# Performance work log

Hardware: AMD Instinct MI355X
Metric: run time of the kernel (lower is better)

## Reference

```python
import jax, jax.numpy as jnp
import numpy as np

N = 50000      # total nodes across batch of molecules
E = 1200000    # directed edges
D_IN = 9       # ESOL num_features
D = 64         # EMBEDDING_DIM
G = 1024       # number of graphs in batch


def setup_inputs() -> dict:
    key = jax.random.key(0)
    ks = jax.random.split(key, 13)
    x = jax.random.normal(ks[0], (N, D_IN), jnp.float32)
    edge_index = jax.random.randint(ks[1], (2, E), 0, N, dtype=jnp.int64)
    batch_index = jnp.sort(jax.random.randint(ks[2], (N,), 0, G, dtype=jnp.int64))

    def glorot(k, shape):
        lim = np.sqrt(6.0 / (shape[0] + shape[1])).astype(np.float32)
        return jax.random.uniform(k, shape, jnp.float32, -lim, lim)

    W0 = glorot(ks[3], (D_IN, D)); b0 = jnp.zeros((D,), jnp.float32)
    W1 = glorot(ks[4], (D, D));    b1 = jnp.zeros((D,), jnp.float32)
    W2 = glorot(ks[5], (D, D));    b2 = jnp.zeros((D,), jnp.float32)
    W3 = glorot(ks[6], (D, D));    b3 = jnp.zeros((D,), jnp.float32)
    Wout = glorot(ks[7], (2 * D, 1)); bout = jnp.zeros((1,), jnp.float32)
    return dict(x=x, edge_index=edge_index, batch_index=batch_index,
                W0=W0, b0=b0, W1=W1, b1=b1, W2=W2, b2=b2, W3=W3, b3=b3,
                Wout=Wout, bout=bout)


def _gcn_conv(h, W, b, src, dst, dinv):
    # GCNConv: D^{-1/2} (A + I) D^{-1/2} (h W) + b, with self-loops in degree.
    h = h @ W                                   # [N, D]
    norm = (dinv[src] * dinv[dst])[:, None]     # [E, 1]
    agg = jax.ops.segment_sum(h[src] * norm, dst, num_segments=N)
    agg = agg + h * (dinv * dinv)[:, None]      # self-loop contribution
    return agg + b


def reference(x, edge_index, batch_index, W0, b0, W1, b1, W2, b2, W3, b3, Wout, bout):
    src, dst = edge_index[0], edge_index[1]
    # degree over A + I (self-loops added), as in PyG GCNConv default
    deg = jax.ops.segment_sum(jnp.ones((E,), x.dtype), dst, num_segments=N) + 1.0
    dinv = jax.lax.rsqrt(deg)

    h = jnp.tanh(_gcn_conv(x, W0, b0, src, dst, dinv))
    h = jnp.tanh(_gcn_conv(h, W1, b1, src, dst, dinv))
    h = jnp.tanh(_gcn_conv(h, W2, b2, src, dst, dinv))
    h = jnp.tanh(_gcn_conv(h, W3, b3, src, dst, dinv))

    # global max pool + global mean pool per graph
    gmax = jax.ops.segment_max(h, batch_index, num_segments=G)
    gmax = jnp.where(jnp.isfinite(gmax), gmax, 0.0)   # guard empty segments
    gsum = jax.ops.segment_sum(h, batch_index, num_segments=G)
    cnt = jax.ops.segment_sum(jnp.ones((N,), h.dtype), batch_index, num_segments=G)
    gmean = gsum / jnp.maximum(cnt, 1.0)[:, None]

    hidden = jnp.concatenate([gmax, gmean], axis=1)   # [G, 2D]
    out = hidden @ Wout + bout                        # [G, 1]
    return out, hidden
```

## Files before the change

### kernel.cpp

```cpp
#include <hip/hip_runtime.h>
#include <math.h>

#define D 64

__global__ void k_zero(int* p, int n) {
    int i = blockIdx.x * blockDim.x + threadIdx.x;
    if (i < n) p[i] = 0;
}

__global__ void k_hist(const int* __restrict__ dst, int* __restrict__ counts, int e) {
    int i = blockIdx.x * blockDim.x + threadIdx.x;
    if (i < e) atomicAdd(&counts[dst[i]], 1);
}

__global__ void k_dinv(const int* __restrict__ counts, float* __restrict__ dinv, int n) {
    int i = blockIdx.x * blockDim.x + threadIdx.x;
    if (i < n) dinv[i] = rsqrtf((float)counts[i] + 1.0f);
}

__global__ void k_scan1(const int* __restrict__ counts, int* __restrict__ bsums, int n) {
    __shared__ int red[256];
    int i = blockIdx.x * 256 + threadIdx.x;
    red[threadIdx.x] = (i < n) ? counts[i] : 0;
    __syncthreads();
    for (int off = 128; off > 0; off >>= 1) {
        if (threadIdx.x < off) red[threadIdx.x] += red[threadIdx.x + off];
        __syncthreads();
    }
    if (threadIdx.x == 0) bsums[blockIdx.x] = red[0];
}

__global__ void k_scan2(int* __restrict__ bsums, int* __restrict__ rowptr, int nb, int n) {
    __shared__ int part[1024];
    int t = threadIdx.x;
    part[t] = (t < nb) ? bsums[t] : 0;
    __syncthreads();
    for (int off = 1; off < 1024; off <<= 1) {
        int v = (t >= off) ? part[t - off] : 0;
        __syncthreads();
        part[t] += v;
        __syncthreads();
    }
    if (t < nb) bsums[t] = (t == 0) ? 0 : part[t - 1];
    if (t == 1023) rowptr[n] = part[1023];
}

__global__ void k_scan3(int* __restrict__ counts, const int* __restrict__ bsums,
                        int* __restrict__ rowptr, int n) {
    __shared__ int part[256];
    int i = blockIdx.x * 256 + threadIdx.x;
    int t = threadIdx.x;
    int v = (i < n) ? counts[i] : 0;
    part[t] = v;
    __syncthreads();
    for (int off = 1; off < 256; off <<= 1) {
        int u = (t >= off) ? part[t - off] : 0;
        __syncthreads();
        part[t] += u;
        __syncthreads();
    }
    if (i < n) {
        int excl = bsums[blockIdx.x] + part[t] - v;
        rowptr[i] = excl;
        counts[i] = excl;
    }
}

__global__ void k_scatter(const int* __restrict__ src, const int* __restrict__ dst,
                          int* __restrict__ cur, int* __restrict__ ssrc, int e) {
    int i = blockIdx.x * blockDim.x + threadIdx.x;
    if (i < e) { int p = atomicAdd(&cur[dst[i]], 1); ssrc[p] = src[i]; }
}

template <int K>
__global__ void k_matmul(const float* __restrict__ h, const float* __restrict__ W,
                         const float* __restrict__ dinv, float* __restrict__ hws, int n) {
    __shared__ float sW[K * D];
    for (int i = threadIdx.x; i < K * D; i += blockDim.x) sW[i] = W[i];
    __syncthreads();
    int col = threadIdx.x & 63;
    int row = blockIdx.x * (blockDim.x >> 6) + (threadIdx.x >> 6);
    if (row >= n) return;
    const float* hr = h + (long)row * K;
    float acc = 0.0f;
#pragma unroll
    for (int k = 0; k < K; ++k) acc = fmaf(hr[k], sW[k * D + col], acc);
    hws[row * D + col] = acc * dinv[row];
}

__global__ void k_aggregate(const int* __restrict__ rowptr, const int* __restrict__ ssrc,
                            const float* __restrict__ dinv, const float* __restrict__ hws,
                            const float* __restrict__ b, float* __restrict__ hout, int n) {
    int node = blockIdx.x * (blockDim.x >> 6) + (threadIdx.x >> 6);
    int lane = threadIdx.x & 63;
    if (node >= n) return;
    int beg = rowptr[node], end = rowptr[node + 1];
    float acc = hws[node * D + lane];
    int e = beg;
    for (; e + 4 <= end; e += 4) {
        int s0 = ssrc[e], s1 = ssrc[e + 1], s2 = ssrc[e + 2], s3 = ssrc[e + 3];
        float a0 = hws[s0 * D + lane], a1 = hws[s1 * D + lane];
        float a2 = hws[s2 * D + lane], a3 = hws[s3 * D + lane];
        acc += a0; acc += a1; acc += a2; acc += a3;
    }
    for (; e < end; ++e) acc += hws[ssrc[e] * D + lane];
    hout[node * D + lane] = tanhf(acc * dinv[node] + b[lane]);
}

__global__ void k_pool(const float* __restrict__ h, const int* __restrict__ batch,
                       const float* __restrict__ Wout, const float* __restrict__ bout,
                       float* __restrict__ out, float* __restrict__ hidden, int n) {
    int g = blockIdx.x;
    int lo = 0, hi = n;
    while (lo < hi) { int mid = (lo + hi) >> 1; if (batch[mid] < g) lo = mid + 1; else hi = mid; }
    int start = lo;
    hi = n;
    while (lo < hi) { int mid = (lo + hi) >> 1; if (batch[mid] < g + 1) lo = mid + 1; else hi = mid; }
    int end = lo;

    int j = threadIdx.x;
    float mx = -INFINITY, sm = 0.0f;
    for (int nd = start; nd < end; ++nd) {
        float v = h[nd * D + j];
        mx = fmaxf(mx, v);
        sm += v;
    }
    float gmax  = (end > start) ? mx : 0.0f;
    float gmean = sm / fmaxf((float)(end - start), 1.0f);

    hidden[g * 2 * D + j]     = gmax;
    hidden[g * 2 * D + D + j] = gmean;

    float p = gmax * Wout[j] + gmean * Wout[D + j];
#pragma unroll
    for (int off = 32; off > 0; off >>= 1) p += __shfl_down(p, off, 64);
    if (j == 0) out[g] = p + bout[0];
}

extern "C" void kernel_launch(void* const* d_in, const int* in_sizes, int n_in,
                              void* d_out, int out_size, void* d_ws, size_t ws_size,
                              hipStream_t stream) {
    const float* x     = (const float*)d_in[0];
    const int*   ei    = (const int*)d_in[1];
    const int*   batch = (const int*)d_in[2];
    const float* W0 = (const float*)d_in[3];  const float* b0 = (const float*)d_in[4];
    const float* W1 = (const float*)d_in[5];  const float* b1 = (const float*)d_in[6];
    const float* W2 = (const float*)d_in[7];  const float* b2 = (const float*)d_in[8];
    const float* W3 = (const float*)d_in[9];  const float* b3 = (const float*)d_in[10];
    const float* Wout = (const float*)d_in[11];
    const float* bout = (const float*)d_in[12];
    float* out = (float*)d_out;

    const int N = in_sizes[0] / 9;
    const int E = in_sizes[1] / 2;
    const int G = out_size / (2 * D + 1);
    const int* src = ei;
    const int* dst = ei + E;
    float* hidden = out + G;

    char* ws = (char*)d_ws;
    size_t off = 0;
    auto alloc = [&](size_t bytes) { void* p = ws + off; off += (bytes + 255) & ~(size_t)255; return p; };
    int*   counts = (int*)alloc((size_t)N * sizeof(int));
    int*   rowptr = (int*)alloc((size_t)(N + 1) * sizeof(int));
    float* dinv   = (float*)alloc((size_t)N * sizeof(float));
    int*   ssrc   = (int*)alloc((size_t)E * sizeof(int));
    int*   bsums  = (int*)alloc(1024 * sizeof(int));
    float* buf0   = (float*)alloc((size_t)N * D * sizeof(float));
    float* buf1   = (float*)alloc((size_t)N * D * sizeof(float));

    const int T = 256;
    const int nb = (N + 255) / 256;

    k_zero<<<(N + T - 1) / T, T, 0, stream>>>(counts, N);
    k_hist<<<(E + T - 1) / T, T, 0, stream>>>(dst, counts, E);
    k_dinv<<<(N + T - 1) / T, T, 0, stream>>>(counts, dinv, N);
    k_scan1<<<nb, 256, 0, stream>>>(counts, bsums, N);
    k_scan2<<<1, 1024, 0, stream>>>(bsums, rowptr, nb, N);
    k_scan3<<<nb, 256, 0, stream>>>(counts, bsums, rowptr, N);
    k_scatter<<<(E + T - 1) / T, T, 0, stream>>>(src, dst, counts, ssrc, E);

    auto layer = [&](const float* hin, int K, const float* W, const float* b) {
        if (K == 9)
            k_matmul<9><<<(N + 3) / 4, T, 0, stream>>>(hin, W, dinv, buf1, N);
        else
            k_matmul<64><<<(N + 3) / 4, T, 0, stream>>>(hin, W, dinv, buf1, N);
        k_aggregate<<<(N + 3) / 4, T, 0, stream>>>(rowptr, ssrc, dinv, buf1, b, buf0, N);
    };

    layer(x,    9,  W0, b0);
    layer(buf0, 64, W1, b1);
    layer(buf0, 64, W2, b2);
    layer(buf0, 64, W3, b3);

    k_pool<<<G, 64, 0, stream>>>(buf0, batch, Wout, bout, out, hidden, N);
}
```

Measured before the change: 601.3 us.

## Build CSR via two-pass LSD radix sort of packed 16-bit dst/src keys

Replaces the atomic histogram plus atomic scatter CSR build with a stable two-pass 8-bit LSD radix sort over edges packed as (dst<<16)|src in 32-bit words. Row pointers come from a binary search on the sorted keys, and degrees are derived from them. The aggregation kernel unpacks src from the low 16 bits. The aim is to replace global atomics on random destinations with workgroup-local histograms and ballot-based ranking, and to give sorted, ordered source lists that may improve gather locality. The packing only holds when N fits in 16 bits, which N=50000 does, and the sort adds several kernel launches.

```diff
diff --git a/kernel.cpp b/kernel.cpp
--- a/kernel.cpp
+++ b/kernel.cpp
@@ -2,26 +2,34 @@
 #include <math.h>
 
 #define D 64
-
-__global__ void k_zero(int* p, int n) {
-    int i = blockIdx.x * blockDim.x + threadIdx.x;
-    if (i < n) p[i] = 0;
-}
-
-__global__ void k_hist(const int* __restrict__ dst, int* __restrict__ counts, int e) {
-    int i = blockIdx.x * blockDim.x + threadIdx.x;
-    if (i < e) atomicAdd(&counts[dst[i]], 1);
-}
-
-__global__ void k_dinv(const int* __restrict__ counts, float* __restrict__ dinv, int n) {
-    int i = blockIdx.x * blockDim.x + threadIdx.x;
-    if (i < n) dinv[i] = rsqrtf((float)counts[i] + 1.0f);
-}
-
-__global__ void k_scan1(const int* __restrict__ counts, int* __restrict__ bsums, int n) {
+#define CHUNK 8192
+#define WAVE_E 2048
+#define ITER 32
+
+
+template <int SHIFT, bool PACKED>
+__global__ void k_rhist(const void* __restrict__ keysrc, int* __restrict__ gmat,
+                        int e, int nwg) {
+    __shared__ int hist[256];
+    int t = threadIdx.x, wg = blockIdx.x;
+    hist[t] = 0;
+    __syncthreads();
+    int base = wg * CHUNK;
+    int lim = min(CHUNK, e - base);
+    for (int i = t; i < lim; i += 256) {
+        unsigned int key;
+        if (PACKED) key = ((const unsigned int*)keysrc)[base + i] >> 16;
+        else        key = (unsigned int)((const int*)keysrc)[base + i];
+        atomicAdd(&hist[(key >> SHIFT) & 255], 1);
+    }
+    __syncthreads();
+    gmat[t * nwg + wg] = hist[t];
+}
+
+__global__ void k_scanA(const int* __restrict__ a, int* __restrict__ bsums, int n) {
     __shared__ int red[256];
     int i = blockIdx.x * 256 + threadIdx.x;
-    red[threadIdx.x] = (i < n) ? counts[i] : 0;
+    red[threadIdx.x] = (i < n) ? a[i] : 0;
     __syncthreads();
     for (int off = 128; off > 0; off >>= 1) {
         if (threadIdx.x < off) red[threadIdx.x] += red[threadIdx.x + off];
@@ -29,8 +37,7 @@
     }
     if (threadIdx.x == 0) bsums[blockIdx.x] = red[0];
 }
-
-__global__ void k_scan2(int* __restrict__ bsums, int* __restrict__ rowptr, int nb, int n) {
+__global__ void k_scanB(int* __restrict__ bsums, int nb) {
     __shared__ int part[1024];
     int t = threadIdx.x;
     part[t] = (t < nb) ? bsums[t] : 0;
@@ -42,15 +49,12 @@
         __syncthreads();
     }
     if (t < nb) bsums[t] = (t == 0) ? 0 : part[t - 1];
-    if (t == 1023) rowptr[n] = part[1023];
-}
-
-__global__ void k_scan3(int* __restrict__ counts, const int* __restrict__ bsums,
-                        int* __restrict__ rowptr, int n) {
+}
+__global__ void k_scanC(int* __restrict__ a, const int* __restrict__ bsums, int n) {
     __shared__ int part[256];
     int i = blockIdx.x * 256 + threadIdx.x;
     int t = threadIdx.x;
-    int v = (i < n) ? counts[i] : 0;
+    int v = (i < n) ? a[i] : 0;
     part[t] = v;
     __syncthreads();
     for (int off = 1; off < 256; off <<= 1) {
@@ -59,17 +63,79 @@
         part[t] += u;
         __syncthreads();
     }
-    if (i < n) {
-        int excl = bsums[blockIdx.x] + part[t] - v;
-        rowptr[i] = excl;
-        counts[i] = excl;
-    }
-}
-
-__global__ void k_scatter(const int* __restrict__ src, const int* __restrict__ dst,
-                          int* __restrict__ cur, int* __restrict__ ssrc, int e) {
+    if (i < n) a[i] = bsums[blockIdx.x] + part[t] - v;
+}
+
+template <int SHIFT>
+__global__ void k_rscat(const int* __restrict__ src, const int* __restrict__ dst,
+                        const unsigned int* __restrict__ inp, const int* __restrict__ gmat,
+                        unsigned int* __restrict__ outp, int e, int nwg) {
+    __shared__ int whist[4][256];
+    __shared__ int cnt[4][256];
+    int t = threadIdx.x, wg = blockIdx.x;
+    int wave = t >> 6, lane = t & 63;
+    for (int w = 0; w < 4; ++w) whist[w][t] = 0;
+    __syncthreads();
+    int qbase = wg * CHUNK + wave * WAVE_E;
+    for (int it = 0; it < ITER; ++it) {
+        int idx = qbase + it * 64 + lane;
+        if (idx < e) {
+            unsigned int w32 = (SHIFT == 0)
+                ? (((unsigned int)dst[idx] << 16) | (unsigned int)src[idx])
+                : inp[idx];
+            atomicAdd(&whist[wave][(w32 >> (16 + SHIFT)) & 255], 1);
+        }
+    }
+    __syncthreads();
+    {
+        int g = gmat[t * nwg + wg];
+        cnt[0][t] = g;
+        g += whist[0][t]; cnt[1][t] = g;
+        g += whist[1][t]; cnt[2][t] = g;
+        g += whist[2][t]; cnt[3][t] = g;
+    }
+    __syncthreads();
+    for (int it = 0; it < ITER; ++it) {
+        int idx = qbase + it * 64 + lane;
+        bool valid = idx < e;
+        unsigned int w32 = 0; int bin = 0;
+        if (valid) {
+            w32 = (SHIFT == 0)
+                ? (((unsigned int)dst[idx] << 16) | (unsigned int)src[idx])
+                : inp[idx];
+            bin = (w32 >> (16 + SHIFT)) & 255;
+        }
+        unsigned long long same = ~0ULL;
+        for (int b = 0; b < 8; ++b) {
+            unsigned long long vote = __ballot((bin >> b) & 1);
+            same &= ((bin >> b) & 1) ? vote : ~vote;
+        }
+        same &= __ballot(valid);
+        if (valid) {
+            int leader = __ffsll(same) - 1;
+            int rank = __popcll(same & ((1ULL << lane) - 1));
+            int old = 0;
+            if (lane == leader) old = atomicAdd(&cnt[wave][bin], (int)__popcll(same));
+            old = __shfl(old, leader, 64);
+            outp[old + rank] = w32;
+        }
+    }
+}
+
+__global__ void k_rowptr(const unsigned int* __restrict__ sp, int* __restrict__ rowptr,
+                         int n, int e) {
+    int d = blockIdx.x * blockDim.x + threadIdx.x;
+    if (d > n) return;
+    if (d == n) { rowptr[n] = e; return; }
+    unsigned int ud = (unsigned int)d;
+    int lo = 0, hi = e;
+    while (lo < hi) { int m = (lo + hi) >> 1; if ((sp[m] >> 16) < ud) lo = m + 1; else hi = m; }
+    rowptr[d] = lo;
+}
+
+__global__ void k_dinv2(const int* __restrict__ rowptr, float* __restrict__ dinv, int n) {
     int i = blockIdx.x * blockDim.x + threadIdx.x;
-    if (i < e) { int p = atomicAdd(&cur[dst[i]], 1); ssrc[p] = src[i]; }
+    if (i < n) dinv[i] = rsqrtf((float)(rowptr[i + 1] - rowptr[i]) + 1.0f);
 }
 
 template <int K>
@@ -88,7 +154,7 @@
     hws[row * D + col] = acc * dinv[row];
 }
 
-__global__ void k_aggregate(const int* __restrict__ rowptr, const int* __restrict__ ssrc,
+__global__ void k_aggregate(const int* __restrict__ rowptr, const unsigned int* __restrict__ sp,
                             const float* __restrict__ dinv, const float* __restrict__ hws,
                             const float* __restrict__ b, float* __restrict__ hout, int n) {
     int node = blockIdx.x * (blockDim.x >> 6) + (threadIdx.x >> 6);
@@ -98,12 +164,13 @@
     float acc = hws[node * D + lane];
     int e = beg;
     for (; e + 4 <= end; e += 4) {
-        int s0 = ssrc[e], s1 = ssrc[e + 1], s2 = ssrc[e + 2], s3 = ssrc[e + 3];
+        int s0 = sp[e] & 0xFFFF, s1 = sp[e + 1] & 0xFFFF;
+        int s2 = sp[e + 2] & 0xFFFF, s3 = sp[e + 3] & 0xFFFF;
         float a0 = hws[s0 * D + lane], a1 = hws[s1 * D + lane];
         float a2 = hws[s2 * D + lane], a3 = hws[s3 * D + lane];
         acc += a0; acc += a1; acc += a2; acc += a3;
     }
-    for (; e < end; ++e) acc += hws[ssrc[e] * D + lane];
+    for (; e < end; ++e) acc += hws[(sp[e] & 0xFFFF) * D + lane];
     hout[node * D + lane] = tanhf(acc * dinv[node] + b[lane]);
 }
 
@@ -158,34 +225,45 @@
     const int* dst = ei + E;
     float* hidden = out + G;
 
+    const int nwg  = (E + CHUNK - 1) / CHUNK;
+    const int glen = 256 * nwg;
+    const int nbg  = (glen + 255) / 256;
+
     char* ws = (char*)d_ws;
     size_t off = 0;
     auto alloc = [&](size_t bytes) { void* p = ws + off; off += (bytes + 255) & ~(size_t)255; return p; };
-    int*   counts = (int*)alloc((size_t)N * sizeof(int));
-    int*   rowptr = (int*)alloc((size_t)(N + 1) * sizeof(int));
-    float* dinv   = (float*)alloc((size_t)N * sizeof(float));
-    int*   ssrc   = (int*)alloc((size_t)E * sizeof(int));
-    int*   bsums  = (int*)alloc(1024 * sizeof(int));
-    float* buf0   = (float*)alloc((size_t)N * D * sizeof(float));
-    float* buf1   = (float*)alloc((size_t)N * D * sizeof(float));
+    unsigned int* bufB  = (unsigned int*)alloc((size_t)E * 4);
+    int*   gmat   = (int*)alloc((size_t)glen * 4);
+    int*   bsums  = (int*)alloc(1024 * 4);
+    int*   rowptr = (int*)alloc((size_t)(N + 1) * 4);
+    float* dinv   = (float*)alloc((size_t)N * 4);
+    float* buf1   = (float*)alloc((size_t)N * D * 4);
+    float* buf0   = (float*)alloc((size_t)N * D * 4);
+    unsigned int* bufA = (unsigned int*)buf0;
 
     const int T = 256;
-    const int nb = (N + 255) / 256;
-
-    k_zero<<<(N + T - 1) / T, T, 0, stream>>>(counts, N);
-    k_hist<<<(E + T - 1) / T, T, 0, stream>>>(dst, counts, E);
-    k_dinv<<<(N + T - 1) / T, T, 0, stream>>>(counts, dinv, N);
-    k_scan1<<<nb, 256, 0, stream>>>(counts, bsums, N);
-    k_scan2<<<1, 1024, 0, stream>>>(bsums, rowptr, nb, N);
-    k_scan3<<<nb, 256, 0, stream>>>(counts, bsums, rowptr, N);
-    k_scatter<<<(E + T - 1) / T, T, 0, stream>>>(src, dst, counts, ssrc, E);
+
+    k_rhist<0, false><<<nwg, 256, 0, stream>>>(dst, gmat, E, nwg);
+    k_scanA<<<nbg, 256, 0, stream>>>(gmat, bsums, glen);
+    k_scanB<<<1, 1024, 0, stream>>>(bsums, nbg);
+    k_scanC<<<nbg, 256, 0, stream>>>(gmat, bsums, glen);
+    k_rscat<0><<<nwg, 256, 0, stream>>>(src, dst, nullptr, gmat, bufA, E, nwg);
+
+    k_rhist<8, true><<<nwg, 256, 0, stream>>>(bufA, gmat, E, nwg);
+    k_scanA<<<nbg, 256, 0, stream>>>(gmat, bsums, glen);
+    k_scanB<<<1, 1024, 0, stream>>>(bsums, nbg);
+    k_scanC<<<nbg, 256, 0, stream>>>(gmat, bsums, glen);
+    k_rscat<8><<<nwg, 256, 0, stream>>>(nullptr, nullptr, bufA, gmat, bufB, E, nwg);
+
+    k_rowptr<<<(N + 1 + T - 1) / T, T, 0, stream>>>(bufB, rowptr, N, E);
+    k_dinv2<<<(N + T - 1) / T, T, 0, stream>>>(rowptr, dinv, N);
 
     auto layer = [&](const float* hin, int K, const float* W, const float* b) {
         if (K == 9)
             k_matmul<9><<<(N + 3) / 4, T, 0, stream>>>(hin, W, dinv, buf1, N);
         else
             k_matmul<64><<<(N + 3) / 4, T, 0, stream>>>(hin, W, dinv, buf1, N);
-        k_aggregate<<<(N + 3) / 4, T, 0, stream>>>(rowptr, ssrc, dinv, buf1, b, buf0, N);
+        k_aggregate<<<(N + 3) / 4, T, 0, stream>>>(rowptr, bufB, dinv, buf1, b, buf0, N);
     };
 
     layer(x,    9,  W0, b0);
```

New measurement: 542.1 us. -9.8%, faster.
